# Kernel optimization log

Measured on AMD Instinct MI355X. Metric: run time of the kernel, lower is better.

## Reference

```python
import jax, jax.numpy as jnp
import numpy as np

N, K, D = 524288, 32, 8
EPS = 1e-6


def setup_inputs() -> dict:
    key = jax.random.key(0)
    k1, k2, k3, k4 = jax.random.split(key, 4)
    x = jax.random.normal(k1, (N, D), dtype=jnp.float32)
    pi = jax.random.uniform(k2, (K,), dtype=jnp.float32)
    means = jax.random.normal(k3, (K, D), dtype=jnp.float32)
    # eye + small perturbation keeps tril(chol_var) well-conditioned (PD covariance)
    chol_var = jnp.eye(D, dtype=jnp.float32)[None] + 0.1 * jax.random.normal(k4, (K, D, D), dtype=jnp.float32)
    return {"x": x, "pi": pi, "means": means, "chol_var": chol_var}


def reference(x, pi, means, chol_var):
    d = x.shape[-1]
    L = jnp.tril(chol_var)                                   # [K,d,d]
    cov = jnp.einsum('kij,klj->kil', L, L) + EPS * jnp.eye(d, dtype=x.dtype)
    C = jnp.linalg.cholesky(cov)                             # [K,d,d] (MVN recomputes cholesky)
    logdet = 2.0 * jnp.sum(jnp.log(jnp.diagonal(C, axis1=-2, axis2=-1)), axis=-1)  # [K]
    eye = jnp.eye(d, dtype=x.dtype)
    Cinv = jax.vmap(lambda c: jax.scipy.linalg.solve_triangular(c, eye, lower=True))(C)  # [K,d,d]
    zx = jnp.einsum('kij,nj->nki', Cinv, x)                  # [N,K,d]
    zm = jnp.einsum('kij,kj->ki', Cinv, means)               # [K,d]
    maha = jnp.sum((zx - zm[None]) ** 2, axis=-1)            # [N,K]
    log_2pi = jnp.log(2.0 * jnp.pi).astype(x.dtype)
    log_probs = -0.5 * (maha + d * log_2pi + logdet[None])   # [N,K]
    wll = log_probs + jax.nn.log_softmax(pi)[None]
    return jax.scipy.special.logsumexp(wll, axis=1)          # [N]
```

## Files before the change

### kernel.cpp

```cpp
#include <hip/hip_runtime.h>
#include <math.h>

#define K_ 32
#define D_ 8
#define NF 48
#define NTHREADS 256
#define NBLOCKS 1024
#define TPW 4

typedef _Float16 half8 __attribute__((ext_vector_type(8)));
typedef float f32x16 __attribute__((ext_vector_type(16)));


__global__ void gmm_prep(
    const float* __restrict__ pi,
    const float* __restrict__ means,
    const float* __restrict__ chol,
    _Float16* __restrict__ wsV)
{
    const int k = threadIdx.x;
    if (k >= K_) return;

    float M[D_][D_];
    {
        const float4* cp = (const float4*)(chol + k * 64);
#pragma unroll
        for (int i = 0; i < D_; ++i) {
            float4 a = cp[2 * i];
            M[i][0] = a.x; M[i][1] = a.y; M[i][2] = a.z; M[i][3] = a.w;
            if (i >= 4) {
                float4 bq = cp[2 * i + 1];
                M[i][4] = bq.x; M[i][5] = bq.y; M[i][6] = bq.z; M[i][7] = bq.w;
            }
        }
    }

    float rd[D_];
#pragma unroll
    for (int i = 0; i < D_; ++i) rd[i] = 1.f / M[i][i];

    float logdet = 0.f;
#pragma unroll
    for (int i = 0; i < D_; ++i) logdet += __logf(fabsf(rd[i]));
    logdet *= -2.f;

#pragma unroll
    for (int j = 0; j < D_; ++j) {
        M[j][j] = rd[j];
#pragma unroll
        for (int i = j + 1; i < D_; ++i) {
            float s = 0.f;
#pragma unroll
            for (int mm = j; mm < i; ++mm) s += M[i][mm] * M[mm][j];
            M[i][j] = -s * rd[i];
        }
    }

#pragma unroll
    for (int i = 0; i < D_; ++i) {
        float t[D_];
#pragma unroll
        for (int j = 0; j <= i; ++j) {
            float s = 0.f;
#pragma unroll
            for (int mm = i; mm < D_; ++mm) s += M[mm][i] * M[mm][j];
            t[j] = s;
        }
#pragma unroll
        for (int j = 0; j <= i; ++j) M[i][j] = t[j];
    }

    float b[D_], q = 0.f;
    {
        const float4* mp = (const float4*)(means + k * 8);
        float4 ma = mp[0], mb = mp[1];
        float mu[D_] = {ma.x, ma.y, ma.z, ma.w, mb.x, mb.y, mb.z, mb.w};
#pragma unroll
        for (int i = 0; i < D_; ++i) {
            float s = 0.f;
#pragma unroll
            for (int j = 0; j <= i; ++j) s += M[i][j] * mu[j];
#pragma unroll
            for (int j = i + 1; j < D_; ++j) s += M[j][i] * mu[j];
            b[i] = s;
            q += s * mu[i];
        }
    }

    float lse;
    {
        float mx = pi[0];
#pragma unroll
        for (int t = 1; t < K_; ++t) mx = fmaxf(mx, pi[t]);
        float se = 0.f;
#pragma unroll
        for (int t = 0; t < K_; ++t) se += __expf(pi[t] - mx);
        lse = mx + __logf(se);
    }

    const float LOG2PI = 1.8378770664093453f;
    const float LOG2E  = 1.4426950408889634f;
    const float ALPHA  = 0.72134752044448170f;
    float cst2 = ((pi[k] - lse) - 0.5f * (logdet + 8.f * LOG2PI)) * LOG2E;

    float V[NF];
    {
        int t = 0;
#pragma unroll
        for (int i = 0; i < D_; ++i)
#pragma unroll
            for (int j = 0; j <= i; ++j)
                V[t++] = (i == j) ? -ALPHA * M[i][i] : -2.f * ALPHA * M[i][j];
#pragma unroll
        for (int i = 0; i < D_; ++i) V[36 + i] = 2.f * ALPHA * b[i];
        V[44] = cst2 - ALPHA * q;
        V[45] = 0.f; V[46] = 0.f; V[47] = 0.f;
    }

#pragma unroll
    for (int s = 0; s < 3; ++s)
#pragma unroll
        for (int h = 0; h < 2; ++h) {
            half8 hv;
#pragma unroll
            for (int j = 0; j < 8; ++j) hv[j] = (_Float16)V[16 * s + 8 * h + j];
            *(half8*)&wsV[(s * 64 + h * 32 + k) * 8] = hv;
        }
}

__global__ __launch_bounds__(NTHREADS) void gmm_mfma(
    const float* __restrict__ x,
    const _Float16* __restrict__ wsV,
    float* __restrict__ out)
{
    const int tid  = threadIdx.x;
    const int lane = tid & 63;
    const int m    = lane & 31;
    const bool h1  = lane >= 32;

    const int w  = blockIdx.x * (NTHREADS / 64) + (tid >> 6);
    const int t0 = w * TPW;
    const float4* xp = (const float4*)x;
    const float LN2 = 0.69314718055994531f;

    float xv[TPW][D_];
#pragma unroll
    for (int u = 0; u < TPW; ++u) {
        const int n = (t0 + u) * 32 + m;
        float4 a = xp[2 * n], b2 = xp[2 * n + 1];
        xv[u][0] = a.x;  xv[u][1] = a.y;  xv[u][2] = a.z;  xv[u][3] = a.w;
        xv[u][4] = b2.x; xv[u][5] = b2.y; xv[u][6] = b2.z; xv[u][7] = b2.w;
    }

    const half8* wp = (const half8*)wsV;
    half8 wf[3];
#pragma unroll
    for (int s = 0; s < 3; ++s) wf[s] = wp[s * 64 + lane];

#pragma unroll
    for (int u = 0; u < TPW; ++u) {
        float Y[NF];
        {
            int t = 0;
#pragma unroll
            for (int i = 0; i < D_; ++i)
#pragma unroll
                for (int j = 0; j <= i; ++j) Y[t++] = xv[u][i] * xv[u][j];
#pragma unroll
            for (int i = 0; i < D_; ++i) Y[36 + i] = xv[u][i];
            Y[44] = 1.f; Y[45] = 0.f; Y[46] = 0.f; Y[47] = 0.f;
        }

        f32x16 acc;
#pragma unroll
        for (int r = 0; r < 16; ++r) acc[r] = 0.f;

#pragma unroll
        for (int s = 0; s < 3; ++s) {
            half8 bf;
#pragma unroll
            for (int j = 0; j < 8; ++j) {
                float v = h1 ? Y[16 * s + 8 + j] : Y[16 * s + j];
                bf[j] = (_Float16)v;
            }
            acc = __builtin_amdgcn_mfma_f32_32x32x16_f16(wf[s], bf, acc, 0, 0, 0);
        }

        float tot = 0.f;
#pragma unroll
        for (int r = 0; r < 16; ++r) tot += exp2f(acc[r]);
        tot += __shfl_xor(tot, 32, 64);
        float res = log2f(tot) * LN2;
        if (!h1) out[(t0 + u) * 32 + m] = res;
    }
}

extern "C" void kernel_launch(void* const* d_in, const int* in_sizes, int n_in,
                              void* d_out, int out_size, void* d_ws, size_t ws_size,
                              hipStream_t stream) {
    const float* x     = (const float*)d_in[0];
    const float* pi    = (const float*)d_in[1];
    const float* means = (const float*)d_in[2];
    const float* chol  = (const float*)d_in[3];
    float* out = (float*)d_out;
    _Float16* wsV = (_Float16*)d_ws;
    (void)in_sizes; (void)n_in; (void)out_size; (void)ws_size;

    gmm_prep<<<1, 64, 0, stream>>>(pi, means, chol, wsV);
    gmm_mfma<<<NBLOCKS, NTHREADS, 0, stream>>>(x, wsV, out);
}
```

Measured before the change: 74.79 us.

## Use full symmetric quadratic feature layout to simplify per-lane B-operand construction

Replaces the packed 45-term upper-triangular feature vector with a full 8x8 outer-product layout (80 features, 5 MFMAs instead of 3). Each lane now builds its B fragments directly as x_i * x_j products with packed fp16 conversions, avoiding the lane-dependent selects over a 48-element Y array. The exp2 reduction is also rewritten as a balanced tree. The cost is two extra MFMA instructions per tile, in exchange for less VALU work and lower register pressure when building operands.

```diff
diff --git a/kernel.cpp b/kernel.cpp
--- a/kernel.cpp
+++ b/kernel.cpp
@@ -3,12 +3,14 @@
 
 #define K_ 32
 #define D_ 8
-#define NF 48
+#define NF 80
+#define NS 5
 #define NTHREADS 256
 #define NBLOCKS 1024
 #define TPW 4
 
 typedef _Float16 half8 __attribute__((ext_vector_type(8)));
+typedef __fp16 fp16x2 __attribute__((ext_vector_type(2)));
 typedef float f32x16 __attribute__((ext_vector_type(16)));
 
 
@@ -104,21 +106,19 @@
     float cst2 = ((pi[k] - lse) - 0.5f * (logdet + 8.f * LOG2PI)) * LOG2E;
 
     float V[NF];
-    {
-        int t = 0;
-#pragma unroll
-        for (int i = 0; i < D_; ++i)
-#pragma unroll
-            for (int j = 0; j <= i; ++j)
-                V[t++] = (i == j) ? -ALPHA * M[i][i] : -2.f * ALPHA * M[i][j];
-#pragma unroll
-        for (int i = 0; i < D_; ++i) V[36 + i] = 2.f * ALPHA * b[i];
-        V[44] = cst2 - ALPHA * q;
-        V[45] = 0.f; V[46] = 0.f; V[47] = 0.f;
-    }
-
-#pragma unroll
-    for (int s = 0; s < 3; ++s)
+#pragma unroll
+    for (int i = 0; i < D_; ++i)
+#pragma unroll
+        for (int j = 0; j < D_; ++j)
+            V[8 * i + j] = -ALPHA * ((i >= j) ? M[i][j] : M[j][i]);
+#pragma unroll
+    for (int j = 0; j < D_; ++j) V[64 + j] = 2.f * ALPHA * b[j];
+    V[72] = cst2 - ALPHA * q;
+#pragma unroll
+    for (int j = 73; j < NF; ++j) V[j] = 0.f;
+
+#pragma unroll
+    for (int s = 0; s < NS; ++s)
 #pragma unroll
         for (int h = 0; h < 2; ++h) {
             half8 hv;
@@ -153,42 +153,56 @@
     }
 
     const half8* wp = (const half8*)wsV;
-    half8 wf[3];
-#pragma unroll
-    for (int s = 0; s < 3; ++s) wf[s] = wp[s * 64 + lane];
+    half8 wf[NS];
+#pragma unroll
+    for (int s = 0; s < NS; ++s) wf[s] = wp[s * 64 + lane];
+
+    f32x16 zc;
+#pragma unroll
+    for (int r = 0; r < 16; ++r) zc[r] = 0.f;
+    half8 c10;
+#pragma unroll
+    for (int j = 0; j < 8; ++j) c10[j] = (_Float16)((j == 0) ? 1.f : 0.f);
 
 #pragma unroll
     for (int u = 0; u < TPW; ++u) {
-        float Y[NF];
-        {
-            int t = 0;
-#pragma unroll
-            for (int i = 0; i < D_; ++i)
-#pragma unroll
-                for (int j = 0; j <= i; ++j) Y[t++] = xv[u][i] * xv[u][j];
-#pragma unroll
-            for (int i = 0; i < D_; ++i) Y[36 + i] = xv[u][i];
-            Y[44] = 1.f; Y[45] = 0.f; Y[46] = 0.f; Y[47] = 0.f;
-        }
+        half8 bq[4];
+#pragma unroll
+        for (int s = 0; s < 4; ++s) {
+            float bc = h1 ? xv[u][2 * s + 1] : xv[u][2 * s];
+#pragma unroll
+            for (int jp = 0; jp < 4; ++jp) {
+                fp16x2 pk = __builtin_amdgcn_cvt_pkrtz(bc * xv[u][2 * jp],
+                                                       bc * xv[u][2 * jp + 1]);
+                bq[s][2 * jp]     = (_Float16)pk[0];
+                bq[s][2 * jp + 1] = (_Float16)pk[1];
+            }
+        }
+        half8 xh;
+#pragma unroll
+        for (int jp = 0; jp < 4; ++jp) {
+            fp16x2 pk = __builtin_amdgcn_cvt_pkrtz(xv[u][2 * jp], xv[u][2 * jp + 1]);
+            xh[2 * jp]     = (_Float16)pk[0];
+            xh[2 * jp + 1] = (_Float16)pk[1];
+        }
+        half8 bf4 = h1 ? c10 : xh;
 
         f32x16 acc;
-#pragma unroll
-        for (int r = 0; r < 16; ++r) acc[r] = 0.f;
-
-#pragma unroll
-        for (int s = 0; s < 3; ++s) {
-            half8 bf;
-#pragma unroll
-            for (int j = 0; j < 8; ++j) {
-                float v = h1 ? Y[16 * s + 8 + j] : Y[16 * s + j];
-                bf[j] = (_Float16)v;
-            }
-            acc = __builtin_amdgcn_mfma_f32_32x32x16_f16(wf[s], bf, acc, 0, 0, 0);
-        }
-
-        float tot = 0.f;
-#pragma unroll
-        for (int r = 0; r < 16; ++r) tot += exp2f(acc[r]);
+        acc = __builtin_amdgcn_mfma_f32_32x32x16_f16(wf[0], bq[0], zc,  0, 0, 0);
+        acc = __builtin_amdgcn_mfma_f32_32x32x16_f16(wf[1], bq[1], acc, 0, 0, 0);
+        acc = __builtin_amdgcn_mfma_f32_32x32x16_f16(wf[2], bq[2], acc, 0, 0, 0);
+        acc = __builtin_amdgcn_mfma_f32_32x32x16_f16(wf[3], bq[3], acc, 0, 0, 0);
+        acc = __builtin_amdgcn_mfma_f32_32x32x16_f16(wf[4], bf4,   acc, 0, 0, 0);
+
+        float e0 = exp2f(acc[0]),  e1 = exp2f(acc[1]),  e2 = exp2f(acc[2]),  e3 = exp2f(acc[3]);
+        float e4 = exp2f(acc[4]),  e5 = exp2f(acc[5]),  e6 = exp2f(acc[6]),  e7 = exp2f(acc[7]);
+        float e8 = exp2f(acc[8]),  e9 = exp2f(acc[9]),  ea = exp2f(acc[10]), eb = exp2f(acc[11]);
+        float ec = exp2f(acc[12]), ed = exp2f(acc[13]), ee = exp2f(acc[14]), ef = exp2f(acc[15]);
+        float s0 = (e0 + e1) + (e2 + e3);
+        float s1 = (e4 + e5) + (e6 + e7);
+        float s2 = (e8 + e9) + (ea + eb);
+        float s3 = (ec + ed) + (ee + ef);
+        float tot = (s0 + s1) + (s2 + s3);
         tot += __shfl_xor(tot, 32, 64);
         float res = log2f(tot) * LN2;
         if (!h1) out[(t0 + u) * 32 + m] = res;
```

New measurement: 74.67 us. Within noise of the previous version (-0.2%).
